# Kernel optimization log

Hardware: AMD Instinct MI355X
Metric: run time of the kernel (lower is better)

Reference implementation:

```python
import jax, jax.numpy as jnp
import numpy as np

N_ITERATIONS = 3
EPS = 1e-07


def squash(t, axis=-1):
    sqr_norm = jnp.sum(t * t, axis=axis, keepdims=True)
    norm = jnp.sqrt(sqr_norm + EPS)
    return sqr_norm * t / ((1.0 + sqr_norm) * norm)


def setup_inputs() -> dict:
    key = jax.random.key(0)
    B, N_IN, N_OUT, D = 256, 1152, 10, 16
    u_hat = jax.random.normal(key, (B, N_IN, N_OUT, D, 1), dtype=jnp.float32)
    return {"u_hat": u_hat}


def reference(u_hat):
    # u_hat: [B, n_in, n_out, d, 1]
    B, n_in, n_out = u_hat.shape[0], u_hat.shape[1], u_hat.shape[2]
    b = jnp.zeros((B, n_in, n_out, 1, 1), dtype=u_hat.dtype)
    v = None
    for r in range(N_ITERATIONS):
        c = jax.nn.softmax(b, axis=1)                      # softmax over input caps
        s = jnp.sum(c * u_hat, axis=1, keepdims=True)      # [B, 1, n_out, d, 1]
        v = squash(s, axis=-2)                             # squash over capsule dim
        if r < N_ITERATIONS - 1:
            # u_hat^T @ v (broadcast v over input caps): agreement [B, n_in, n_out, 1, 1]
            a = jnp.sum(u_hat * v, axis=-2, keepdims=True)
            b = b + a
    return jnp.squeeze(v, axis=1)                          # [B, n_out, d, 1]
```

## Files before the change

kernel.cpp:

```cpp
#include <hip/hip_runtime.h>

#define BATCH 256
#define NIN   1152
#define NOUT  10
#define DDIM  16
#define KPT   9

__global__ __launch_bounds__(512, 6)
void routing_kernel(const float* __restrict__ u_hat, float* __restrict__ out) {
    __shared__ float bsh[NIN];
    __shared__ float wsh[NIN];
    __shared__ float red[8][DDIM];
    __shared__ float vsh[DDIM];
    __shared__ float smax[8];
    __shared__ float ssum[8];

    const int t    = threadIdx.x;
    const int q    = t & 3;
    const int g    = t >> 2;
    const int wave = t >> 6;
    const int lane = t & 63;

    const int x   = blockIdx.x;
    const int xcd = x & 7;
    const int j   = x >> 3;
    const int oo  = j % NOUT;
    const int bb  = xcd * 32 + j / NOUT;

    const float* base = u_hat + (size_t)bb * (NIN * NOUT * DDIM) + oo * DDIM + q * 4;

    float4 u[KPT];
#pragma unroll
    for (int k = 0; k < KPT; ++k) {
        const int i = g + 128 * k;
        u[k] = *reinterpret_cast<const float4*>(base + (size_t)i * (NOUT * DDIM));
    }

    for (int i = t; i < NIN; i += 512) bsh[i] = 0.0f;
    __syncthreads();

    float scale = 0.0f;
    for (int r = 0; r < 3; ++r) {
        float m = -3.4e38f;
        for (int i = t; i < NIN; i += 512) m = fmaxf(m, bsh[i]);
        for (int off = 32; off >= 1; off >>= 1) m = fmaxf(m, __shfl_down(m, off));
        if (lane == 0) smax[wave] = m;
        __syncthreads();
        m = fmaxf(fmaxf(fmaxf(smax[0], smax[1]), fmaxf(smax[2], smax[3])),
                  fmaxf(fmaxf(smax[4], smax[5]), fmaxf(smax[6], smax[7])));

        float z = 0.0f;
        for (int i = t; i < NIN; i += 512) {
            const float w = __expf(bsh[i] - m);
            wsh[i] = w;
            z += w;
        }
        for (int off = 32; off >= 1; off >>= 1) z += __shfl_down(z, off);
        if (lane == 0) ssum[wave] = z;
        __syncthreads();
        const float invZ = 1.0f / (((ssum[0] + ssum[1]) + (ssum[2] + ssum[3])) +
                                   ((ssum[4] + ssum[5]) + (ssum[6] + ssum[7])));

        float sx = 0.f, sy = 0.f, sz = 0.f, sw = 0.f;
#pragma unroll
        for (int k = 0; k < KPT; ++k) {
            const float w = wsh[g + 128 * k];
            sx += w * u[k].x; sy += w * u[k].y; sz += w * u[k].z; sw += w * u[k].w;
        }
        for (int off = 32; off >= 4; off >>= 1) {
            sx += __shfl_down(sx, off);
            sy += __shfl_down(sy, off);
            sz += __shfl_down(sz, off);
            sw += __shfl_down(sw, off);
        }
        if (lane < 4) {
            float* rp = &red[wave][lane * 4];
            rp[0] = sx; rp[1] = sy; rp[2] = sz; rp[3] = sw;
        }
        __syncthreads();
        if (t < DDIM) {
            vsh[t] = (((red[0][t] + red[1][t]) + (red[2][t] + red[3][t])) +
                      ((red[4][t] + red[5][t]) + (red[6][t] + red[7][t]))) * invZ;
        }
        __syncthreads();

        float sqr = 0.0f;
#pragma unroll
        for (int d = 0; d < DDIM; ++d) { const float sv = vsh[d]; sqr += sv * sv; }
        scale = sqr / ((1.0f + sqr) * sqrtf(sqr + 1e-7f));

        if (r == 2) break;

        const float vx = vsh[q * 4 + 0] * scale, vy = vsh[q * 4 + 1] * scale;
        const float vz = vsh[q * 4 + 2] * scale, vw = vsh[q * 4 + 3] * scale;
#pragma unroll
        for (int k = 0; k < KPT; ++k) {
            float a = u[k].x * vx + u[k].y * vy + u[k].z * vz + u[k].w * vw;
            a += __shfl_xor(a, 1);
            a += __shfl_xor(a, 2);
            if (q == 0) bsh[g + 128 * k] += a;
        }
        __syncthreads();
    }

    if (t < DDIM) {
        out[(size_t)(bb * NOUT + oo) * DDIM + t] = vsh[t] * scale;
    }
}

extern "C" void kernel_launch(void* const* d_in, const int* in_sizes, int n_in,
                              void* d_out, int out_size, void* d_ws, size_t ws_size,
                              hipStream_t stream) {
    const float* u_hat = (const float*)d_in[0];
    float* out = (float*)d_out;
    routing_kernel<<<dim3(BATCH * NOUT), dim3(512), 0, stream>>>(u_hat, out);
}
```

Baseline: 262.1 us.

## Make routing kernel persistent with register double-buffered prefetch of next item

The grid drops from 2560 blocks to 512 persistent blocks, and each block now processes 5 (batch, output-capsule) items in sequence. While routing the current item, the block issues register loads for the next item's u_hat slice into a second register buffer, so global memory latency overlaps with the softmax and agreement compute. Holding two buffers doubles register use for u_hat, and the occupancy hint is lowered from 6 to 4 blocks per CU. Fewer, longer blocks may also balance less evenly across CUs.

```diff
diff --git a/kernel.cpp b/kernel.cpp
--- a/kernel.cpp
+++ b/kernel.cpp
@@ -5,41 +5,31 @@
 #define NOUT  10
 #define DDIM  16
 #define KPT   9
+#define NBLK  512
+#define STEPS 5
 
-__global__ __launch_bounds__(512, 6)
-void routing_kernel(const float* __restrict__ u_hat, float* __restrict__ out) {
-    __shared__ float bsh[NIN];
-    __shared__ float wsh[NIN];
-    __shared__ float red[8][DDIM];
-    __shared__ float vsh[DDIM];
-    __shared__ float smax[8];
-    __shared__ float ssum[8];
 
-    const int t    = threadIdx.x;
-    const int q    = t & 3;
-    const int g    = t >> 2;
-    const int wave = t >> 6;
-    const int lane = t & 63;
-
-    const int x   = blockIdx.x;
-    const int xcd = x & 7;
-    const int j   = x >> 3;
-    const int oo  = j % NOUT;
-    const int bb  = xcd * 32 + j / NOUT;
-
-    const float* base = u_hat + (size_t)bb * (NIN * NOUT * DDIM) + oo * DDIM + q * 4;
-
-    float4 u[KPT];
+__device__ __forceinline__ void route_item(
+    const float4 (&u)[KPT], float4 (&unext)[KPT],
+    const float* __restrict__ next_base, const bool do_prefetch,
+    float* __restrict__ outp,
+    float* bsh, float* wsh, float (*red)[DDIM], float* vsh,
+    float* smax, float* ssum,
+    const int t, const int q, const int g, const int wave, const int lane)
+{
+    if (do_prefetch) {
 #pragma unroll
-    for (int k = 0; k < KPT; ++k) {
-        const int i = g + 128 * k;
-        u[k] = *reinterpret_cast<const float4*>(base + (size_t)i * (NOUT * DDIM));
+        for (int k = 0; k < KPT; ++k) {
+            const int i = g + 128 * k;
+            unext[k] = *reinterpret_cast<const float4*>(next_base + (size_t)i * (NOUT * DDIM));
+        }
     }
 
     for (int i = t; i < NIN; i += 512) bsh[i] = 0.0f;
     __syncthreads();
 
     float scale = 0.0f;
+#pragma unroll 1
     for (int r = 0; r < 3; ++r) {
         float m = -3.4e38f;
         for (int i = t; i < NIN; i += 512) m = fmaxf(m, bsh[i]);
@@ -104,7 +94,62 @@
     }
 
     if (t < DDIM) {
-        out[(size_t)(bb * NOUT + oo) * DDIM + t] = vsh[t] * scale;
+        outp[t] = vsh[t] * scale;
+    }
+}
+
+__global__ __launch_bounds__(512, 4)
+void routing_kernel(const float* __restrict__ u_hat, float* __restrict__ out) {
+    __shared__ float bsh[NIN];
+    __shared__ float wsh[NIN];
+    __shared__ float red[8][DDIM];
+    __shared__ float vsh[DDIM];
+    __shared__ float smax[8];
+    __shared__ float ssum[8];
+
+    const int t    = threadIdx.x;
+    const int q    = t & 3;
+    const int g    = t >> 2;
+    const int wave = t >> 6;
+    const int lane = t & 63;
+
+    const int pb    = blockIdx.x;
+    const int x     = pb & 7;
+    const int local = pb >> 3;
+
+    auto ubase = [&](int s) -> const float* {
+        const int id = s * 64 + local;
+        const int bb = x * 32 + id / 10;
+        const int oo = id % 10;
+        return u_hat + (size_t)bb * (NIN * NOUT * DDIM) + oo * DDIM + q * 4;
+    };
+    auto obase = [&](int s) -> float* {
+        const int id = s * 64 + local;
+        const int bb = x * 32 + id / 10;
+        const int oo = id % 10;
+        return out + (size_t)(bb * NOUT + oo) * DDIM;
+    };
+
+    float4 uA[KPT], uB[KPT];
+
+    {
+        const float* base = ubase(0);
+#pragma unroll
+        for (int k = 0; k < KPT; ++k) {
+            const int i = g + 128 * k;
+            uA[k] = *reinterpret_cast<const float4*>(base + (size_t)i * (NOUT * DDIM));
+        }
+    }
+
+#pragma unroll
+    for (int s = 0; s < STEPS; ++s) {
+        const bool pf = (s + 1 < STEPS);
+        const float* nb = pf ? ubase(s + 1) : nullptr;
+        float* op = obase(s);
+        if (s & 1) route_item(uB, uA, nb, pf, op, bsh, wsh, red, vsh, smax, ssum,
+                              t, q, g, wave, lane);
+        else       route_item(uA, uB, nb, pf, op, bsh, wsh, red, vsh, smax, ssum,
+                              t, q, g, wave, lane);
     }
 }
 
@@ -113,5 +158,5 @@
                               hipStream_t stream) {
     const float* u_hat = (const float*)d_in[0];
     float* out = (float*)d_out;
-    routing_kernel<<<dim3(BATCH * NOUT), dim3(512), 0, stream>>>(u_hat, out);
+    routing_kernel<<<dim3(NBLK), dim3(512), 0, stream>>>(u_hat, out);
 }
```

Measured after the change: 277.0 us. 1.06x slower.

## Keep routing logits in registers and fuse softmax with weighted sum

Applied to the files above, without the earlier changes.

Routing logits b are now held per-thread in registers matching the u_hat fragments instead of shared arrays, so the max, exp and weighted-sum passes use no LDS traffic. The normalizer sum is fused into the weighted-sum reduction and one barrier per iteration is dropped, with raw s_barrier plus lgkmcnt waits replacing __syncthreads. This removes shared-memory round trips and synchronization, at the cost of redundant exp computation across the four lanes of each quad and a few more registers.

```diff
diff --git a/kernel.cpp b/kernel.cpp
--- a/kernel.cpp
+++ b/kernel.cpp
@@ -6,10 +6,15 @@
 #define DDIM  16
 #define KPT   9
 
+
+__device__ __forceinline__ void bar_lds() {
+    asm volatile("s_waitcnt lgkmcnt(0)" ::: "memory");
+    __builtin_amdgcn_s_barrier();
+    asm volatile("" ::: "memory");
+}
+
 __global__ __launch_bounds__(512, 6)
 void routing_kernel(const float* __restrict__ u_hat, float* __restrict__ out) {
-    __shared__ float bsh[NIN];
-    __shared__ float wsh[NIN];
     __shared__ float red[8][DDIM];
     __shared__ float vsh[DDIM];
     __shared__ float smax[8];
@@ -36,53 +41,51 @@
         u[k] = *reinterpret_cast<const float4*>(base + (size_t)i * (NOUT * DDIM));
     }
 
-    for (int i = t; i < NIN; i += 512) bsh[i] = 0.0f;
-    __syncthreads();
+    float b[KPT];
+#pragma unroll
+    for (int k = 0; k < KPT; ++k) b[k] = 0.0f;
 
     float scale = 0.0f;
+#pragma unroll 1
     for (int r = 0; r < 3; ++r) {
-        float m = -3.4e38f;
-        for (int i = t; i < NIN; i += 512) m = fmaxf(m, bsh[i]);
-        for (int off = 32; off >= 1; off >>= 1) m = fmaxf(m, __shfl_down(m, off));
+        float m = b[0];
+#pragma unroll
+        for (int k = 1; k < KPT; ++k) m = fmaxf(m, b[k]);
+        for (int off = 32; off >= 4; off >>= 1) m = fmaxf(m, __shfl_down(m, off));
         if (lane == 0) smax[wave] = m;
-        __syncthreads();
+        bar_lds();
         m = fmaxf(fmaxf(fmaxf(smax[0], smax[1]), fmaxf(smax[2], smax[3])),
                   fmaxf(fmaxf(smax[4], smax[5]), fmaxf(smax[6], smax[7])));
 
         float z = 0.0f;
-        for (int i = t; i < NIN; i += 512) {
-            const float w = __expf(bsh[i] - m);
-            wsh[i] = w;
-            z += w;
-        }
-        for (int off = 32; off >= 1; off >>= 1) z += __shfl_down(z, off);
-        if (lane == 0) ssum[wave] = z;
-        __syncthreads();
-        const float invZ = 1.0f / (((ssum[0] + ssum[1]) + (ssum[2] + ssum[3])) +
-                                   ((ssum[4] + ssum[5]) + (ssum[6] + ssum[7])));
-
         float sx = 0.f, sy = 0.f, sz = 0.f, sw = 0.f;
 #pragma unroll
         for (int k = 0; k < KPT; ++k) {
-            const float w = wsh[g + 128 * k];
-            sx += w * u[k].x; sy += w * u[k].y; sz += w * u[k].z; sw += w * u[k].w;
+            const float wk = __expf(b[k] - m);
+            z  += wk;
+            sx += wk * u[k].x; sy += wk * u[k].y;
+            sz += wk * u[k].z; sw += wk * u[k].w;
         }
         for (int off = 32; off >= 4; off >>= 1) {
+            z  += __shfl_down(z,  off);
             sx += __shfl_down(sx, off);
             sy += __shfl_down(sy, off);
             sz += __shfl_down(sz, off);
             sw += __shfl_down(sw, off);
         }
+        if (lane == 0) ssum[wave] = z;
         if (lane < 4) {
             float* rp = &red[wave][lane * 4];
             rp[0] = sx; rp[1] = sy; rp[2] = sz; rp[3] = sw;
         }
-        __syncthreads();
+        bar_lds();
         if (t < DDIM) {
+            const float invZ = 1.0f / (((ssum[0] + ssum[1]) + (ssum[2] + ssum[3])) +
+                                       ((ssum[4] + ssum[5]) + (ssum[6] + ssum[7])));
             vsh[t] = (((red[0][t] + red[1][t]) + (red[2][t] + red[3][t])) +
                       ((red[4][t] + red[5][t]) + (red[6][t] + red[7][t]))) * invZ;
         }
-        __syncthreads();
+        bar_lds();
 
         float sqr = 0.0f;
 #pragma unroll
@@ -98,9 +101,8 @@
             float a = u[k].x * vx + u[k].y * vy + u[k].z * vz + u[k].w * vw;
             a += __shfl_xor(a, 1);
             a += __shfl_xor(a, 2);
-            if (q == 0) bsh[g + 128 * k] += a;
+            b[k] += a;
         }
-        __syncthreads();
     }
 
     if (t < DDIM) {
```

Result: slower. 311.5 us (+18.9%).
